# Kernel tuning notes

Measured on AMD Instinct MI355X. Metric: run time of the kernel, lower is better.

The kernel has to match this reference:

```python
import jax, jax.numpy as jnp
import numpy as np

EMB = 1024
HEADS = 16
HEAD_DIM = EMB // HEADS
N = 16384


def setup_inputs() -> dict:
    key = jax.random.key(0)
    ks = jax.random.split(key, 9)
    s = 1.0 / np.sqrt(EMB)
    return {
        "src": jax.random.normal(ks[0], (N, EMB), dtype=jnp.float32),
        "Wq": jax.random.normal(ks[1], (EMB, EMB), dtype=jnp.float32) * s,
        "bq": jax.random.normal(ks[2], (EMB,), dtype=jnp.float32) * s,
        "Wk": jax.random.normal(ks[3], (EMB, EMB), dtype=jnp.float32) * s,
        "bk": jax.random.normal(ks[4], (EMB,), dtype=jnp.float32) * s,
        "Wv": jax.random.normal(ks[5], (EMB, EMB), dtype=jnp.float32) * s,
        "bv": jax.random.normal(ks[6], (EMB,), dtype=jnp.float32) * s,
        "Wo": jax.random.normal(ks[7], (EMB, EMB), dtype=jnp.float32) * s,
        "bo": jax.random.normal(ks[8], (EMB,), dtype=jnp.float32) * s,
    }


def reference(src, Wq, bq, Wk, bk, Wv, bv, Wo, bo):
    # nn.Linear: y = x @ W^T + b  (W is [out, in])
    q = src @ Wq.T + bq          # [N, E]
    k = src @ Wk.T + bk
    v = src @ Wv.T + bv
    q = q.reshape(-1, HEADS, HEAD_DIM)   # [N, H, D]
    k = k.reshape(-1, HEADS, HEAD_DIM)
    v = v.reshape(-1, HEADS, HEAD_DIM)
    # NOTE: attention is across heads within each token: scores [N, H, H]
    scale = 1.0 / jnp.sqrt(jnp.float32(HEAD_DIM))
    scores = jnp.einsum('nhd,ngd->nhg', q, k) * scale   # [N, H, H]
    attn = jax.nn.softmax(scores, axis=-1)
    out = jnp.einsum('nhg,ngd->nhd', attn, v)            # [N, H, D]
    out = out.reshape(-1, EMB)
    out = out @ Wo.T + bo                                 # [N, E]
    return out.reshape(-1, HEADS, HEAD_DIM)               # [N, H, D]
```

## Files before the change

### kernel.cpp

```cpp
#include <hip/hip_runtime.h>
#include <stdint.h>
#include <stddef.h>

#define EMB 1024
#define NTOK 16384

typedef __attribute__((ext_vector_type(8))) short short8;
typedef __attribute__((ext_vector_type(4))) float floatx4;

__device__ __forceinline__ unsigned short f2bf(float f) {
    union { float f; unsigned int u; } v; v.f = f;
    unsigned int u = v.u;
    unsigned int r = (u + 0x7fffu + ((u >> 16) & 1u)) >> 16;
    return (unsigned short)r;
}
__device__ __forceinline__ float bf2f(unsigned short s) {
    union { unsigned int u; float f; } v; v.u = ((unsigned int)s) << 16;
    return v.f;
}

__device__ __forceinline__ void gload16(const void* g, void* l) {
    __builtin_amdgcn_global_load_lds(
        (const __attribute__((address_space(1))) void*)g,
        (__attribute__((address_space(3))) void*)l, 16, 0, 0);
}

__global__ void cvt_kernel(const float* __restrict__ in,
                           unsigned short* __restrict__ out, int n4) {
    int idx = blockIdx.x * blockDim.x + threadIdx.x;
    int stride = gridDim.x * blockDim.x;
    for (int i = idx; i < n4; i += stride) {
        float4 f = reinterpret_cast<const float4*>(in)[i];
        ushort4 o;
        o.x = f2bf(f.x); o.y = f2bf(f.y); o.z = f2bf(f.z); o.w = f2bf(f.w);
        reinterpret_cast<ushort4*>(out)[i] = o;
    }
}

__global__ void bias_cat_kernel(const float* __restrict__ b0,
                                const float* __restrict__ b1,
                                const float* __restrict__ b2,
                                float* __restrict__ out) {
    int i = blockIdx.x * blockDim.x + threadIdx.x;
    float v = (i < 1024) ? b0[i] : (i < 2048 ? b1[i - 1024] : b2[i - 2048]);
    out[i] = v;
}

__device__ __forceinline__ void store_val(float* C, size_t idx, float v) { C[idx] = v; }
__device__ __forceinline__ void store_val(unsigned short* C, size_t idx, float v) { C[idx] = f2bf(v); }

template<typename OUT_T>
__global__ __launch_bounds__(512, 2)
void gemm256(const unsigned short* __restrict__ A,
             const unsigned short* __restrict__ B,
             const float* __restrict__ bias,
             OUT_T* __restrict__ C,
             int K, int Nc, int grid_m)
{
    __shared__ unsigned short lds[65536];

    const int bid = blockIdx.x;
    const int cpx = gridDim.x >> 3;
    const int wg  = (bid & 7) * cpx + (bid >> 3);
    const int m0 = (wg % grid_m) * 256;
    const int n0 = (wg / grid_m) * 256;

    const int tid  = threadIdx.x;
    const int lane = tid & 63;
    const int wid  = tid >> 6;
    const int wm = (wid >> 2) * 128;
    const int wn = (wid & 3) * 64;
    const int rr = lane & 15;
    const int klo = (((lane >> 4) ^ ((rr >> 1) & 3)) << 3);

    const unsigned short* pA[2];
    const unsigned short* pB[2];
    int ldst[2];
#pragma unroll
    for (int l = 0; l < 2; ++l) {
        const int P16  = l * 512 + tid;
        const int rowS = P16 >> 2;
        const int colel = (((P16 & 3) ^ ((rowS >> 1) & 3)) << 3);
        pA[l] = A + (size_t)(m0 + rowS) * K + colel;
        pB[l] = B + (size_t)(n0 + rowS) * K + colel;
        ldst[l] = P16 * 8;
    }

    floatx4 acc[8][4];
#pragma unroll
    for (int i = 0; i < 8; ++i)
#pragma unroll
        for (int j = 0; j < 4; ++j)
            acc[i][j] = (floatx4){0.f, 0.f, 0.f, 0.f};

    const int NT = K >> 6;

#pragma unroll
    for (int l = 0; l < 2; ++l) {
        gload16(pA[l],      &lds[0     + ldst[l]]);
        gload16(pA[l] + 32, &lds[8192  + ldst[l]]);
        gload16(pB[l],      &lds[16384 + ldst[l]]);
        gload16(pB[l] + 32, &lds[24576 + ldst[l]]);
    }
    asm volatile("s_waitcnt vmcnt(0)" ::: "memory");
    asm volatile("s_barrier" ::: "memory");

    for (int t = 0; t < NT; ++t) {
        const int cur = (t & 1) * 32768;
        const int nxt = cur ^ 32768;
        const int ktn = (t + 1 < NT) ? (t + 1) * 64 : 0;

        short8 bf[4];

        {
            short8 af[4];
            const unsigned short* la = &lds[cur + (wm + rr) * 32 + klo];
#pragma unroll
            for (int i = 0; i < 4; ++i) af[i] = *reinterpret_cast<const short8*>(la + i * 512);
            const unsigned short* lb = &lds[cur + 16384 + (wn + rr) * 32 + klo];
#pragma unroll
            for (int j = 0; j < 4; ++j) bf[j] = *reinterpret_cast<const short8*>(lb + j * 512);
            gload16(pA[0] + ktn, &lds[nxt + ldst[0]]);
            gload16(pA[1] + ktn, &lds[nxt + ldst[1]]);
            asm volatile("s_barrier" ::: "memory");
            __builtin_amdgcn_s_setprio(1);
#pragma unroll
            for (int j = 0; j < 4; ++j)
#pragma unroll
                for (int i = 0; i < 4; ++i)
                    acc[i][j] = __builtin_amdgcn_mfma_f32_16x16x32_bf16(af[i], bf[j], acc[i][j], 0, 0, 0);
            __builtin_amdgcn_s_setprio(0);
            asm volatile("s_barrier" ::: "memory");
        }
        {
            short8 af[4];
            const unsigned short* la = &lds[cur + (wm + 64 + rr) * 32 + klo];
#pragma unroll
            for (int i = 0; i < 4; ++i) af[i] = *reinterpret_cast<const short8*>(la + i * 512);
            gload16(pB[0] + ktn, &lds[nxt + 16384 + ldst[0]]);
            gload16(pB[1] + ktn, &lds[nxt + 16384 + ldst[1]]);
            asm volatile("s_barrier" ::: "memory");
            __builtin_amdgcn_s_setprio(1);
#pragma unroll
            for (int j = 0; j < 4; ++j)
#pragma unroll
                for (int i = 0; i < 4; ++i)
                    acc[4 + i][j] = __builtin_amdgcn_mfma_f32_16x16x32_bf16(af[i], bf[j], acc[4 + i][j], 0, 0, 0);
            __builtin_amdgcn_s_setprio(0);
            asm volatile("s_waitcnt vmcnt(4)" ::: "memory");
            asm volatile("s_barrier" ::: "memory");
        }
        {
            short8 af[4];
            const unsigned short* la = &lds[cur + 8192 + (wm + rr) * 32 + klo];
#pragma unroll
            for (int i = 0; i < 4; ++i) af[i] = *reinterpret_cast<const short8*>(la + i * 512);
            const unsigned short* lb = &lds[cur + 24576 + (wn + rr) * 32 + klo];
#pragma unroll
            for (int j = 0; j < 4; ++j) bf[j] = *reinterpret_cast<const short8*>(lb + j * 512);
            gload16(pA[0] + ktn + 32, &lds[nxt + 8192 + ldst[0]]);
            gload16(pA[1] + ktn + 32, &lds[nxt + 8192 + ldst[1]]);
            asm volatile("s_barrier" ::: "memory");
            __builtin_amdgcn_s_setprio(1);
#pragma unroll
            for (int j = 0; j < 4; ++j)
#pragma unroll
                for (int i = 0; i < 4; ++i)
                    acc[i][j] = __builtin_amdgcn_mfma_f32_16x16x32_bf16(af[i], bf[j], acc[i][j], 0, 0, 0);
            __builtin_amdgcn_s_setprio(0);
            asm volatile("s_barrier" ::: "memory");
        }
        {
            short8 af[4];
            const unsigned short* la = &lds[cur + 8192 + (wm + 64 + rr) * 32 + klo];
#pragma unroll
            for (int i = 0; i < 4; ++i) af[i] = *reinterpret_cast<const short8*>(la + i * 512);
            gload16(pB[0] + ktn + 32, &lds[nxt + 24576 + ldst[0]]);
            gload16(pB[1] + ktn + 32, &lds[nxt + 24576 + ldst[1]]);
            asm volatile("s_barrier" ::: "memory");
            __builtin_amdgcn_s_setprio(1);
#pragma unroll
            for (int j = 0; j < 4; ++j)
#pragma unroll
                for (int i = 0; i < 4; ++i)
                    acc[4 + i][j] = __builtin_amdgcn_mfma_f32_16x16x32_bf16(af[i], bf[j], acc[4 + i][j], 0, 0, 0);
            __builtin_amdgcn_s_setprio(0);
            asm volatile("s_waitcnt vmcnt(4)" ::: "memory");
            asm volatile("s_barrier" ::: "memory");
        }
    }

    const int cn  = lane & 15;
    const int cm4 = (lane >> 4) * 4;
    float bv[4];
#pragma unroll
    for (int j = 0; j < 4; ++j) bv[j] = bias[n0 + wn + j * 16 + cn];
#pragma unroll
    for (int ai = 0; ai < 8; ++ai) {
        const int row = m0 + wm + (ai >> 2) * 64 + (ai & 3) * 16 + cm4;
#pragma unroll
        for (int j = 0; j < 4; ++j) {
            const int col = n0 + wn + j * 16 + cn;
#pragma unroll
            for (int r = 0; r < 4; ++r)
                store_val(C, (size_t)(row + r) * Nc + col, acc[ai][j][r] + bv[j]);
        }
    }
}

#define ROWP 72

__global__ __launch_bounds__(256)
void attn_kernel(const unsigned short* __restrict__ QKV,
                 unsigned short* __restrict__ O)
{
    const int wave = threadIdx.x >> 6;
    const int lane = threadIdx.x & 63;
    const int n = blockIdx.x * 4 + wave;

    __shared__ unsigned short lq[4][16 * ROWP];
    __shared__ unsigned short lk[4][16 * ROWP];
    __shared__ unsigned short lv[4][16 * ROWP];
    __shared__ float lp[4][256];

    {
        const unsigned short* gq = QKV + (size_t)n * 3072;
        const unsigned short* gk = gq + 1024;
        const unsigned short* gv = gq + 2048;
        for (int t = lane; t < 128; t += 64) {
            int r = t >> 3, c = t & 7;
            *reinterpret_cast<short8*>(&lq[wave][r * ROWP + c * 8]) =
                *reinterpret_cast<const short8*>(gq + t * 8);
            *reinterpret_cast<short8*>(&lk[wave][r * ROWP + c * 8]) =
                *reinterpret_cast<const short8*>(gk + t * 8);
            *reinterpret_cast<short8*>(&lv[wave][r * ROWP + c * 8]) =
                *reinterpret_cast<const short8*>(gv + t * 8);
        }
    }
    __syncthreads();

    const int g = lane & 15;
    const int a = lane >> 4;

    float kf[64];
#pragma unroll
    for (int c2 = 0; c2 < 8; ++c2) {
        short8 kv = *reinterpret_cast<const short8*>(&lk[wave][g * ROWP + c2 * 8]);
#pragma unroll
        for (int e = 0; e < 8; ++e) kf[c2 * 8 + e] = bf2f((unsigned short)kv[e]);
    }

#pragma unroll
    for (int i = 0; i < 4; ++i) {
        const int h = i * 4 + a;
        float s = 0.f;
#pragma unroll
        for (int c2 = 0; c2 < 8; ++c2) {
            short8 qv = *reinterpret_cast<const short8*>(&lq[wave][h * ROWP + c2 * 8]);
#pragma unroll
            for (int e = 0; e < 8; ++e)
                s = fmaf(bf2f((unsigned short)qv[e]), kf[c2 * 8 + e], s);
        }
        s *= 0.125f;

        float m = s;
#pragma unroll
        for (int o = 1; o < 16; o <<= 1) m = fmaxf(m, __shfl_xor(m, o, 64));
        float p = expf(s - m);
        float sum = p;
#pragma unroll
        for (int o = 1; o < 16; o <<= 1) sum += __shfl_xor(sum, o, 64);
        lp[wave][h * 16 + g] = p / sum;
    }
    __syncthreads();

    const int h = lane >> 2;
    const int db = (lane & 3) * 16;
    float o[16];
#pragma unroll
    for (int e = 0; e < 16; ++e) o[e] = 0.f;

    for (int g2 = 0; g2 < 16; ++g2) {
        const float pw = lp[wave][h * 16 + g2];
        short8 v0 = *reinterpret_cast<const short8*>(&lv[wave][g2 * ROWP + db]);
        short8 v1 = *reinterpret_cast<const short8*>(&lv[wave][g2 * ROWP + db + 8]);
#pragma unroll
        for (int e = 0; e < 8; ++e) {
            o[e]     = fmaf(pw, bf2f((unsigned short)v0[e]), o[e]);
            o[8 + e] = fmaf(pw, bf2f((unsigned short)v1[e]), o[8 + e]);
        }
    }

    short8 o0, o1;
#pragma unroll
    for (int e = 0; e < 8; ++e) {
        o0[e] = (short)f2bf(o[e]);
        o1[e] = (short)f2bf(o[8 + e]);
    }
    unsigned short* dst = O + (size_t)n * EMB + h * 64 + db;
    *reinterpret_cast<short8*>(dst) = o0;
    *reinterpret_cast<short8*>(dst + 8) = o1;
}

extern "C" void kernel_launch(void* const* d_in, const int* in_sizes, int n_in,
                              void* d_out, int out_size, void* d_ws, size_t ws_size,
                              hipStream_t stream)
{
    const float* src = (const float*)d_in[0];
    const float* Wq  = (const float*)d_in[1];
    const float* bq  = (const float*)d_in[2];
    const float* Wk  = (const float*)d_in[3];
    const float* bk  = (const float*)d_in[4];
    const float* Wv  = (const float*)d_in[5];
    const float* bv  = (const float*)d_in[6];
    const float* Wo  = (const float*)d_in[7];
    const float* bo  = (const float*)d_in[8];
    float* out = (float*)d_out;

    unsigned short* ws = (unsigned short*)d_ws;
    unsigned short* src_bf = ws;
    unsigned short* wqkv   = src_bf + (size_t)NTOK * EMB;
    unsigned short* wo_bf  = wqkv + (size_t)3 * EMB * EMB;
    unsigned short* qkv    = wo_bf + (size_t)EMB * EMB;
    unsigned short* ab     = qkv + (size_t)NTOK * 3 * EMB;
    float* bias_cat        = (float*)(ab + (size_t)NTOK * EMB);

    cvt_kernel<<<2048, 256, 0, stream>>>(src, src_bf, NTOK * EMB / 4);
    cvt_kernel<<<512, 256, 0, stream>>>(Wq, wqkv,                       EMB * EMB / 4);
    cvt_kernel<<<512, 256, 0, stream>>>(Wk, wqkv + (size_t)EMB * EMB,   EMB * EMB / 4);
    cvt_kernel<<<512, 256, 0, stream>>>(Wv, wqkv + (size_t)2 * EMB * EMB, EMB * EMB / 4);
    cvt_kernel<<<512, 256, 0, stream>>>(Wo, wo_bf, EMB * EMB / 4);
    bias_cat_kernel<<<12, 256, 0, stream>>>(bq, bk, bv, bias_cat);

    gemm256<unsigned short><<<dim3(64 * 12), 512, 0, stream>>>(
        src_bf, wqkv, bias_cat, qkv, EMB, 3 * EMB, 64);

    attn_kernel<<<NTOK / 4, 256, 0, stream>>>(qkv, ab);

    gemm256<float><<<dim3(64 * 4), 512, 0, stream>>>(
        ab, wo_bf, bo, out, EMB, EMB, 64);
}
```

Baseline: 223.7 us.

## Software-pipeline LDS fragment loads in GEMM and merge weight conversion launches

The GEMM main loop is restructured so LDS fragment reads for the next MFMA block are issued before the current block's MFMAs, using ping-pong A and B register fragments. The next tile's first fragments are preloaded at the end of each iteration, which hides LDS latency behind matrix math. Separately, the four weight conversion launches are merged into one kernel that writes contiguously, relying on wo_bf directly following wqkv in the workspace. The cost is higher register pressure from the doubled fragment registers and a changed barrier ordering, which could affect correctness or occupancy.

Result: no change. 227.5 us (+1.7%).

```diff
diff --git a/kernel.cpp b/kernel.cpp
--- a/kernel.cpp
+++ b/kernel.cpp
@@ -37,6 +37,22 @@
     }
 }
 
+__global__ void cvt4_kernel(const float* __restrict__ s0, const float* __restrict__ s1,
+                            const float* __restrict__ s2, const float* __restrict__ s3,
+                            unsigned short* __restrict__ out) {
+    int idx = blockIdx.x * blockDim.x + threadIdx.x;
+    const int total = 4 << 18;
+    int stride = gridDim.x * blockDim.x;
+    for (int i = idx; i < total; i += stride) {
+        int w = i >> 18, r = i & ((1 << 18) - 1);
+        const float* s = (w == 0) ? s0 : (w == 1) ? s1 : (w == 2) ? s2 : s3;
+        float4 f = reinterpret_cast<const float4*>(s)[r];
+        ushort4 o;
+        o.x = f2bf(f.x); o.y = f2bf(f.y); o.z = f2bf(f.z); o.w = f2bf(f.w);
+        reinterpret_cast<ushort4*>(out)[i] = o;
+    }
+}
+
 __global__ void bias_cat_kernel(const float* __restrict__ b0,
                                 const float* __restrict__ b1,
                                 const float* __restrict__ b2,
@@ -105,89 +121,86 @@
     asm volatile("s_waitcnt vmcnt(0)" ::: "memory");
     asm volatile("s_barrier" ::: "memory");
 
+    short8 afA[4], afB[4], bfA[4], bfB[4];
+#pragma unroll
+    for (int i = 0; i < 4; ++i)
+        afA[i] = *reinterpret_cast<const short8*>(&lds[(wm + i * 16 + rr) * 32 + klo]);
+#pragma unroll
+    for (int j = 0; j < 4; ++j)
+        bfA[j] = *reinterpret_cast<const short8*>(&lds[16384 + (wn + j * 16 + rr) * 32 + klo]);
+
     for (int t = 0; t < NT; ++t) {
         const int cur = (t & 1) * 32768;
         const int nxt = cur ^ 32768;
         const int ktn = (t + 1 < NT) ? (t + 1) * 64 : 0;
 
-        short8 bf[4];
-
-        {
-            short8 af[4];
-            const unsigned short* la = &lds[cur + (wm + rr) * 32 + klo];
-#pragma unroll
-            for (int i = 0; i < 4; ++i) af[i] = *reinterpret_cast<const short8*>(la + i * 512);
-            const unsigned short* lb = &lds[cur + 16384 + (wn + rr) * 32 + klo];
-#pragma unroll
-            for (int j = 0; j < 4; ++j) bf[j] = *reinterpret_cast<const short8*>(lb + j * 512);
-            gload16(pA[0] + ktn, &lds[nxt + ldst[0]]);
-            gload16(pA[1] + ktn, &lds[nxt + ldst[1]]);
-            asm volatile("s_barrier" ::: "memory");
-            __builtin_amdgcn_s_setprio(1);
-#pragma unroll
-            for (int j = 0; j < 4; ++j)
-#pragma unroll
-                for (int i = 0; i < 4; ++i)
-                    acc[i][j] = __builtin_amdgcn_mfma_f32_16x16x32_bf16(af[i], bf[j], acc[i][j], 0, 0, 0);
-            __builtin_amdgcn_s_setprio(0);
-            asm volatile("s_barrier" ::: "memory");
-        }
-        {
-            short8 af[4];
-            const unsigned short* la = &lds[cur + (wm + 64 + rr) * 32 + klo];
-#pragma unroll
-            for (int i = 0; i < 4; ++i) af[i] = *reinterpret_cast<const short8*>(la + i * 512);
-            gload16(pB[0] + ktn, &lds[nxt + 16384 + ldst[0]]);
-            gload16(pB[1] + ktn, &lds[nxt + 16384 + ldst[1]]);
-            asm volatile("s_barrier" ::: "memory");
-            __builtin_amdgcn_s_setprio(1);
-#pragma unroll
-            for (int j = 0; j < 4; ++j)
-#pragma unroll
-                for (int i = 0; i < 4; ++i)
-                    acc[4 + i][j] = __builtin_amdgcn_mfma_f32_16x16x32_bf16(af[i], bf[j], acc[4 + i][j], 0, 0, 0);
-            __builtin_amdgcn_s_setprio(0);
-            asm volatile("s_waitcnt vmcnt(4)" ::: "memory");
-            asm volatile("s_barrier" ::: "memory");
-        }
-        {
-            short8 af[4];
-            const unsigned short* la = &lds[cur + 8192 + (wm + rr) * 32 + klo];
-#pragma unroll
-            for (int i = 0; i < 4; ++i) af[i] = *reinterpret_cast<const short8*>(la + i * 512);
-            const unsigned short* lb = &lds[cur + 24576 + (wn + rr) * 32 + klo];
-#pragma unroll
-            for (int j = 0; j < 4; ++j) bf[j] = *reinterpret_cast<const short8*>(lb + j * 512);
-            gload16(pA[0] + ktn + 32, &lds[nxt + 8192 + ldst[0]]);
-            gload16(pA[1] + ktn + 32, &lds[nxt + 8192 + ldst[1]]);
-            asm volatile("s_barrier" ::: "memory");
-            __builtin_amdgcn_s_setprio(1);
-#pragma unroll
-            for (int j = 0; j < 4; ++j)
-#pragma unroll
-                for (int i = 0; i < 4; ++i)
-                    acc[i][j] = __builtin_amdgcn_mfma_f32_16x16x32_bf16(af[i], bf[j], acc[i][j], 0, 0, 0);
-            __builtin_amdgcn_s_setprio(0);
-            asm volatile("s_barrier" ::: "memory");
-        }
-        {
-            short8 af[4];
-            const unsigned short* la = &lds[cur + 8192 + (wm + 64 + rr) * 32 + klo];
-#pragma unroll
-            for (int i = 0; i < 4; ++i) af[i] = *reinterpret_cast<const short8*>(la + i * 512);
-            gload16(pB[0] + ktn + 32, &lds[nxt + 24576 + ldst[0]]);
-            gload16(pB[1] + ktn + 32, &lds[nxt + 24576 + ldst[1]]);
-            asm volatile("s_barrier" ::: "memory");
-            __builtin_amdgcn_s_setprio(1);
-#pragma unroll
-            for (int j = 0; j < 4; ++j)
-#pragma unroll
-                for (int i = 0; i < 4; ++i)
-                    acc[4 + i][j] = __builtin_amdgcn_mfma_f32_16x16x32_bf16(af[i], bf[j], acc[4 + i][j], 0, 0, 0);
-            __builtin_amdgcn_s_setprio(0);
-            asm volatile("s_waitcnt vmcnt(4)" ::: "memory");
-            asm volatile("s_barrier" ::: "memory");
-        }
+        gload16(pA[0] + ktn, &lds[nxt + ldst[0]]);
+        gload16(pA[1] + ktn, &lds[nxt + ldst[1]]);
+#pragma unroll
+        for (int i = 0; i < 4; ++i)
+            afB[i] = *reinterpret_cast<const short8*>(&lds[cur + (wm + 64 + i * 16 + rr) * 32 + klo]);
+        asm volatile("s_barrier" ::: "memory");
+        __builtin_amdgcn_s_setprio(1);
+#pragma unroll
+        for (int j = 0; j < 4; ++j)
+#pragma unroll
+            for (int i = 0; i < 4; ++i)
+                acc[i][j] = __builtin_amdgcn_mfma_f32_16x16x32_bf16(afA[i], bfA[j], acc[i][j], 0, 0, 0);
+        __builtin_amdgcn_s_setprio(0);
+        asm volatile("s_barrier" ::: "memory");
+
+        gload16(pB[0] + ktn, &lds[nxt + 16384 + ldst[0]]);
+        gload16(pB[1] + ktn, &lds[nxt + 16384 + ldst[1]]);
+        asm volatile("s_waitcnt vmcnt(4)" ::: "memory");
+        asm volatile("s_barrier" ::: "memory");
+#pragma unroll
+        for (int i = 0; i < 4; ++i)
+            afA[i] = *reinterpret_cast<const short8*>(&lds[cur + 8192 + (wm + i * 16 + rr) * 32 + klo]);
+#pragma unroll
+        for (int j = 0; j < 4; ++j)
+            bfB[j] = *reinterpret_cast<const short8*>(&lds[cur + 24576 + (wn + j * 16 + rr) * 32 + klo]);
+        __builtin_amdgcn_s_setprio(1);
+#pragma unroll
+        for (int j = 0; j < 4; ++j)
+#pragma unroll
+            for (int i = 0; i < 4; ++i)
+                acc[4 + i][j] = __builtin_amdgcn_mfma_f32_16x16x32_bf16(afB[i], bfA[j], acc[4 + i][j], 0, 0, 0);
+        __builtin_amdgcn_s_setprio(0);
+        asm volatile("s_barrier" ::: "memory");
+
+        gload16(pA[0] + ktn + 32, &lds[nxt + 8192 + ldst[0]]);
+        gload16(pA[1] + ktn + 32, &lds[nxt + 8192 + ldst[1]]);
+#pragma unroll
+        for (int i = 0; i < 4; ++i)
+            afB[i] = *reinterpret_cast<const short8*>(&lds[cur + 8192 + (wm + 64 + i * 16 + rr) * 32 + klo]);
+        asm volatile("s_barrier" ::: "memory");
+        __builtin_amdgcn_s_setprio(1);
+#pragma unroll
+        for (int j = 0; j < 4; ++j)
+#pragma unroll
+            for (int i = 0; i < 4; ++i)
+                acc[i][j] = __builtin_amdgcn_mfma_f32_16x16x32_bf16(afA[i], bfB[j], acc[i][j], 0, 0, 0);
+        __builtin_amdgcn_s_setprio(0);
+        asm volatile("s_barrier" ::: "memory");
+
+        gload16(pB[0] + ktn + 32, &lds[nxt + 24576 + ldst[0]]);
+        gload16(pB[1] + ktn + 32, &lds[nxt + 24576 + ldst[1]]);
+        asm volatile("s_waitcnt vmcnt(4)" ::: "memory");
+        asm volatile("s_barrier" ::: "memory");
+#pragma unroll
+        for (int i = 0; i < 4; ++i)
+            afA[i] = *reinterpret_cast<const short8*>(&lds[nxt + (wm + i * 16 + rr) * 32 + klo]);
+#pragma unroll
+        for (int j = 0; j < 4; ++j)
+            bfA[j] = *reinterpret_cast<const short8*>(&lds[nxt + 16384 + (wn + j * 16 + rr) * 32 + klo]);
+        __builtin_amdgcn_s_setprio(1);
+#pragma unroll
+        for (int j = 0; j < 4; ++j)
+#pragma unroll
+            for (int i = 0; i < 4; ++i)
+                acc[4 + i][j] = __builtin_amdgcn_mfma_f32_16x16x32_bf16(afB[i], bfB[j], acc[4 + i][j], 0, 0, 0);
+        __builtin_amdgcn_s_setprio(0);
+        asm volatile("s_barrier" ::: "memory");
     }
 
     const int cn  = lane & 15;
@@ -326,10 +339,7 @@
     float* bias_cat        = (float*)(ab + (size_t)NTOK * EMB);
 
     cvt_kernel<<<2048, 256, 0, stream>>>(src, src_bf, NTOK * EMB / 4);
-    cvt_kernel<<<512, 256, 0, stream>>>(Wq, wqkv,                       EMB * EMB / 4);
-    cvt_kernel<<<512, 256, 0, stream>>>(Wk, wqkv + (size_t)EMB * EMB,   EMB * EMB / 4);
-    cvt_kernel<<<512, 256, 0, stream>>>(Wv, wqkv + (size_t)2 * EMB * EMB, EMB * EMB / 4);
-    cvt_kernel<<<512, 256, 0, stream>>>(Wo, wo_bf, EMB * EMB / 4);
+    cvt4_kernel<<<2048, 256, 0, stream>>>(Wq, Wk, Wv, Wo, wqkv);
     bias_cat_kernel<<<12, 256, 0, stream>>>(bq, bk, bv, bias_cat);
 
     gemm256<unsigned short><<<dim3(64 * 12), 512, 0, stream>>>(
```
